# Optimization experiments

Hardware: AMD Instinct MI355X
Metric: run time of the kernel (lower is better)

Reference implementation:

```python
import jax, jax.numpy as jnp
import numpy as np

B, L, PD, DIM, H, DH, DEPTH, MLP, NIMG, NCLS, TH = 2, 2048, 768, 512, 8, 64, 2, 2048, 4, 1000, 32


def _ln(x, g):
    # bias-free LayerNorm (beta buffer is zeros), eps matches torch F.layer_norm
    mu = jnp.mean(x, axis=-1, keepdims=True)
    var = jnp.var(x, axis=-1, keepdims=True)
    return (x - mu) / jnp.sqrt(var + 1e-5) * g


def _rms(x, g):
    # F.normalize(dim=-1) * sqrt(dim_head) * gamma; x: [b,h,n,dh], g: [h,1,dh]
    n = jnp.linalg.norm(x, axis=-1, keepdims=True)
    return x / jnp.maximum(n, 1e-12) * (DH ** 0.5) * g


def _attn(x, context, mask, ln_g, qg, kg, Wq, Wkv, Wo):
    b, n = x.shape[0], x.shape[1]
    xn = _ln(x, ln_g)
    kv = xn if context is None else context  # context is NOT pre-normed (matches source)
    m = kv.shape[1]
    q = (xn @ Wq).reshape(b, n, H, DH).transpose(0, 2, 1, 3)   # [b,h,n,dh]
    k, v = jnp.split(kv @ Wkv, 2, axis=-1)
    k = k.reshape(b, m, H, DH).transpose(0, 2, 1, 3)
    v = v.reshape(b, m, H, DH).transpose(0, 2, 1, 3)
    q = _rms(q, qg)
    k = _rms(k, kg)
    dots = jnp.einsum('bhid,bhjd->bhij', q, k)  # no 1/sqrt(d): QK-RMSNorm carries the scale
    neg = -jnp.finfo(dots.dtype).max
    dots = jnp.where(mask, dots, neg)
    a = jax.nn.softmax(dots, axis=-1)
    out = jnp.einsum('bhij,bhjd->bhid', a, v)
    out = out.transpose(0, 2, 1, 3).reshape(b, n, H * DH)
    return out @ Wo


def _forward(patches, ln_pe1_g, W_pe, b_pe, ln_pe2_g, pos_h_emb, pos_w_emb,
             attn_ln_g, q_g, k_g, Wq, Wkv, Wo, ff_ln_g, W1, b1, W2, b2,
             final_ln_g, pool_q, pool_ln_g, pool_q_g, pool_k_g,
             pool_Wq, pool_Wkv, pool_Wo, head_ln_g, W_head,
             pos_h, pos_w, image_ids):
    # patch embedding: LN -> Linear -> LN, then factorized 2D pos embed
    x = _ln(patches, ln_pe1_g) @ W_pe + b_pe
    x = _ln(x, ln_pe2_g)
    x = x + pos_h_emb[pos_h] + pos_w_emb[pos_w]
    # block-diagonal attention mask: tokens attend only within their image
    mask = (image_ids[:, None, :, None] == image_ids[:, None, None, :])  # [B,1,L,L]
    for i in range(DEPTH):
        x = _attn(x, None, mask, attn_ln_g[i], q_g[i], k_g[i], Wq[i], Wkv[i], Wo[i]) + x
        h = _ln(x, ff_ln_g[i]) @ W1[i] + b1[i]
        h = jax.nn.gelu(h, approximate=False)
        x = h @ W2[i] + b2[i] + x
    x = _ln(x, final_ln_g)
    # attention pooling: one learned query per packed image
    queries = jnp.broadcast_to(pool_q, (B, NIMG, DIM))
    pmask = (jnp.arange(NIMG)[None, None, :, None] == image_ids[:, None, None, :])  # [B,1,NIMG,L]
    pooled = _attn(queries, x, pmask, pool_ln_g, pool_q_g, pool_k_g, pool_Wq, pool_Wkv, pool_Wo) + queries
    return _ln(pooled, head_ln_g) @ W_head  # [B, NIMG, NCLS]


def setup_inputs() -> dict:
    key = jax.random.key(0)
    ks = jax.random.split(key, 16)
    s = 0.02
    inp = {}
    inp['patches'] = jax.random.normal(ks[0], (B, L, PD), jnp.float32)
    inp['pos_h'] = jax.random.randint(ks[1], (B, L), 0, TH)
    inp['pos_w'] = jax.random.randint(ks[2], (B, L), 0, TH)
    inp['image_ids'] = jnp.sort(jax.random.randint(ks[3], (B, L), 0, NIMG), axis=-1)
    inp['ln_pe1_g'] = jnp.ones((PD,), jnp.float32)
    inp['W_pe'] = jax.random.normal(ks[4], (PD, DIM), jnp.float32) * s
    inp['b_pe'] = jnp.zeros((DIM,), jnp.float32)
    inp['ln_pe2_g'] = jnp.ones((DIM,), jnp.float32)
    inp['pos_h_emb'] = jax.random.normal(ks[5], (TH, DIM), jnp.float32)
    inp['pos_w_emb'] = jax.random.normal(ks[6], (TH, DIM), jnp.float32)
    inp['attn_ln_g'] = jnp.ones((DEPTH, DIM), jnp.float32)
    inp['q_g'] = jnp.ones((DEPTH, H, 1, DH), jnp.float32)
    inp['k_g'] = jnp.ones((DEPTH, H, 1, DH), jnp.float32)
    inp['Wq'] = jax.random.normal(ks[7], (DEPTH, DIM, H * DH), jnp.float32) * s
    inp['Wkv'] = jax.random.normal(ks[8], (DEPTH, DIM, 2 * H * DH), jnp.float32) * s
    inp['Wo'] = jax.random.normal(ks[9], (DEPTH, H * DH, DIM), jnp.float32) * s
    inp['ff_ln_g'] = jnp.ones((DEPTH, DIM), jnp.float32)
    inp['W1'] = jax.random.normal(ks[10], (DEPTH, DIM, MLP), jnp.float32) * s
    inp['b1'] = jnp.zeros((DEPTH, MLP), jnp.float32)
    inp['W2'] = jax.random.normal(ks[11], (DEPTH, MLP, DIM), jnp.float32) * s
    inp['b2'] = jnp.zeros((DEPTH, DIM), jnp.float32)
    inp['final_ln_g'] = jnp.ones((DIM,), jnp.float32)
    inp['pool_q'] = jax.random.normal(ks[12], (DIM,), jnp.float32)
    inp['pool_ln_g'] = jnp.ones((DIM,), jnp.float32)
    inp['pool_q_g'] = jnp.ones((H, 1, DH), jnp.float32)
    inp['pool_k_g'] = jnp.ones((H, 1, DH), jnp.float32)
    inp['pool_Wq'] = jax.random.normal(ks[13], (DIM, H * DH), jnp.float32) * s
    inp['pool_Wkv'] = jax.random.normal(ks[14], (DIM, 2 * H * DH), jnp.float32) * s
    inp['pool_Wo'] = jax.random.normal(ks[15], (H * DH, DIM), jnp.float32) * s
    inp['head_ln_g'] = jnp.ones((DIM,), jnp.float32)
    inp['W_head'] = jax.random.normal(jax.random.fold_in(key, 99), (DIM, NCLS), jnp.float32) * s
    return inp


def reference(patches, pos_h, pos_w, image_ids, ln_pe1_g, W_pe, b_pe, ln_pe2_g,
              pos_h_emb, pos_w_emb, attn_ln_g, q_g, k_g, Wq, Wkv, Wo, ff_ln_g,
              W1, b1, W2, b2, final_ln_g, pool_q, pool_ln_g, pool_q_g, pool_k_g,
              pool_Wq, pool_Wkv, pool_Wo, head_ln_g, W_head):
    return _forward(patches, ln_pe1_g, W_pe, b_pe, ln_pe2_g, pos_h_emb, pos_w_emb,
                    attn_ln_g, q_g, k_g, Wq, Wkv, Wo, ff_ln_g, W1, b1, W2, b2,
                    final_ln_g, pool_q, pool_ln_g, pool_q_g, pool_k_g,
                    pool_Wq, pool_Wkv, pool_Wo, head_ln_g, W_head,
                    pos_h, pos_w, image_ids)
```

## Files before the change

kernel.cpp:

```cpp
#include <hip/hip_runtime.h>
#include <hip/hip_bf16.h>
#include <cfloat>
#include <math.h>

#define BB 2
#define LL 2048
#define PD 768
#define DIM 512
#define HH 8
#define DH 64
#define DEPTH 2
#define MLP 2048
#define NIMG 4
#define NCLS 1000
#define ROWS (BB*LL)
#define QKV (3*DIM)
#define NEGBIG (-1e30f)

typedef __hip_bfloat16 bf16;
typedef __bf16 v8bf __attribute__((ext_vector_type(8)));
typedef float f32x4 __attribute__((ext_vector_type(4)));

__device__ __forceinline__ float ldin(const void* p, size_t i, int bf) {
    return bf ? __bfloat162float(((const bf16*)p)[i]) : ((const float*)p)[i];
}
__device__ __forceinline__ float lda(const float* p, size_t i) { return p[i]; }
__device__ __forceinline__ float lda(const bf16* p, size_t i) { return __bfloat162float(p[i]); }
__device__ __forceinline__ void st(float* p, size_t i, float v) { p[i] = v; }
__device__ __forceinline__ void st(bf16* p, size_t i, float v) { p[i] = __float2bfloat16(v); }
__device__ __forceinline__ unsigned short f2bf(float x) {
    return __builtin_bit_cast(unsigned short, __float2bfloat16(x));
}
__device__ __forceinline__ float us2f(unsigned short u) {
    return __bfloat162float(__builtin_bit_cast(bf16, u));
}

__device__ __forceinline__ void stage16(const void* gsrc, void* ldst)
{
    __builtin_amdgcn_global_load_lds(
        (const __attribute__((address_space(1))) unsigned int*)(unsigned long long)gsrc,
        (__attribute__((address_space(3))) unsigned int*)(unsigned int)(unsigned long long)ldst,
        16, 0, 0);
}

__global__ void detect_dtype_kernel(const void* ones, int* flag)
{
    if (threadIdx.x == 0 && blockIdx.x == 0)
        *flag = (((const unsigned*)ones)[0] == 0x3F803F80u) ? 1 : 0;
}

__global__ void wconv_kernel(const void* __restrict__ W, int K, int N, size_t inStride,
                             bf16* __restrict__ out, size_t outOff, size_t outStride,
                             const int* dtf)
{
    __shared__ float t[32][33];
    const int bf = *dtf;
    const size_t zin = (size_t)blockIdx.z * inStride;
    const size_t zout = outOff + (size_t)blockIdx.z * outStride;
    const int kb = blockIdx.y * 32, nb = blockIdx.x * 32;
    const int tx = threadIdx.x, ty = threadIdx.y;
    #pragma unroll
    for (int u = 0; u < 4; ++u)
        t[ty + 8 * u][tx] = ldin(W, zin + (size_t)(kb + ty + 8 * u) * N + nb + tx, bf);
    __syncthreads();
    #pragma unroll
    for (int u = 0; u < 4; ++u)
        out[zout + (size_t)(nb + ty + 8 * u) * K + kb + tx] = __float2bfloat16(t[tx][ty + 8 * u]);
}

template<int RAWIN, typename TOUT>
__global__ void ln_kernel(const void* __restrict__ in, const void* __restrict__ g, size_t goff,
                          TOUT* __restrict__ out, int D, const int* dtf)
{
    __shared__ float red[16];
    const int bf = *dtf;
    const int row = blockIdx.x, tid = threadIdx.x;
    const size_t base = (size_t)row * D;
    float s = 0.f, ss = 0.f;
    for (int d = tid; d < D; d += blockDim.x) {
        float v = RAWIN ? ldin(in, base + d, bf) : ((const float*)in)[base + d];
        s += v; ss += v * v;
    }
    for (int o = 32; o; o >>= 1) { s += __shfl_xor(s, o); ss += __shfl_xor(ss, o); }
    const int wid = tid >> 6, lane = tid & 63, nw = blockDim.x >> 6;
    if (lane == 0) { red[wid] = s; red[8 + wid] = ss; }
    __syncthreads();
    if (tid == 0) {
        float a = 0.f, b = 0.f;
        for (int w = 0; w < nw; ++w) { a += red[w]; b += red[8 + w]; }
        red[0] = a; red[8] = b;
    }
    __syncthreads();
    const float mean = red[0] / D;
    const float var  = red[8] / D - mean * mean;
    const float rstd = rsqrtf(var + 1e-5f);
    for (int d = tid; d < D; d += blockDim.x) {
        float v = RAWIN ? ldin(in, base + d, bf) : ((const float*)in)[base + d];
        st(out, base + d, (v - mean) * rstd * ldin(g, goff + d, bf));
    }
}

__global__ void patch_fuse_kernel(const float* __restrict__ part,
                                  const void* __restrict__ b_pe,
                                  const void* __restrict__ g1,
                                  const void* __restrict__ phe, const void* __restrict__ pwe,
                                  const int* __restrict__ ph, const int* __restrict__ pw,
                                  const void* __restrict__ g2,
                                  float* __restrict__ x, bf16* __restrict__ xb,
                                  const int* dtf)
{
    __shared__ float red[16];
    const int bf = *dtf;
    const int row = blockIdx.x, tid = threadIdx.x;
    const size_t base = (size_t)row * DIM;
    const int wid = tid >> 6, lane = tid & 63;
    float v[2];
    float s = 0.f, ss = 0.f;
    #pragma unroll
    for (int u = 0; u < 2; ++u) {
        const int d = tid + 256 * u;
        float a = part[base + d] + part[(size_t)ROWS * DIM + base + d] + ldin(b_pe, d, bf);
        v[u] = a; s += a; ss += a * a;
    }
    for (int o = 32; o; o >>= 1) { s += __shfl_xor(s, o); ss += __shfl_xor(ss, o); }
    if (lane == 0) { red[wid] = s; red[8 + wid] = ss; }
    __syncthreads();
    if (tid == 0) {
        float a = 0.f, b = 0.f;
        for (int w2 = 0; w2 < 4; ++w2) { a += red[w2]; b += red[8 + w2]; }
        red[0] = a; red[8] = b;
    }
    __syncthreads();
    {
        const float mean = red[0] / DIM;
        const float var  = red[8] / DIM - mean * mean;
        const float rstd = rsqrtf(var + 1e-5f);
        const size_t hoff = (size_t)ph[row] * DIM, woff = (size_t)pw[row] * DIM;
        s = 0.f; ss = 0.f;
        #pragma unroll
        for (int u = 0; u < 2; ++u) {
            const int d = tid + 256 * u;
            float a = (v[u] - mean) * rstd * ldin(g1, d, bf)
                    + ldin(phe, hoff + d, bf) + ldin(pwe, woff + d, bf);
            x[base + d] = a;
            v[u] = a; s += a; ss += a * a;
        }
    }
    for (int o = 32; o; o >>= 1) { s += __shfl_xor(s, o); ss += __shfl_xor(ss, o); }
    __syncthreads();
    if (lane == 0) { red[wid] = s; red[8 + wid] = ss; }
    __syncthreads();
    if (tid == 0) {
        float a = 0.f, b = 0.f;
        for (int w2 = 0; w2 < 4; ++w2) { a += red[w2]; b += red[8 + w2]; }
        red[0] = a; red[8] = b;
    }
    __syncthreads();
    const float mean = red[0] / DIM;
    const float var  = red[8] / DIM - mean * mean;
    const float rstd = rsqrtf(var + 1e-5f);
    #pragma unroll
    for (int u = 0; u < 2; ++u) {
        const int d = tid + 256 * u;
        xb[base + d] = __float2bfloat16((v[u] - mean) * rstd * ldin(g2, d, bf));
    }
}

#define GM 128
#define GN 64
#define GK 64

template<typename TO, int EPI>
__global__ void mgemm_kernel(const bf16* __restrict__ A, const bf16* __restrict__ Wt,
                             const void* __restrict__ bias, size_t boff,
                             const float* __restrict__ resid, TO* __restrict__ out,
                             int M, int N, int K, int kc, int gelu, const int* dtf)
{
    __shared__ __align__(16) unsigned short As[2][GM][GK];
    __shared__ __align__(16) unsigned short Bs[2][GN][GK];
    const int tid = threadIdx.x;
    const int w = tid >> 6, l = tid & 63, g = l >> 4, c = l & 15;
    const int wm = (w >> 1) * 64, wn = (w & 1) * 32;
    const int m0 = blockIdx.y * GM, n0 = blockIdx.x * GN;
    const int kbeg = blockIdx.z * kc;
    const int lrow = l >> 3, lcol = (l & 7) * 8;

#define STAGE_MG(BUF, K0)                                                          \
    {                                                                              \
        _Pragma("unroll")                                                          \
        for (int u = 0; u < 4; ++u) {                                              \
            const int rr = 32 * w + 8 * u;                                         \
            stage16(A + (size_t)(m0 + rr + lrow) * K + (K0) + lcol, &As[BUF][rr][0]); \
        }                                                                          \
        _Pragma("unroll")                                                          \
        for (int u = 0; u < 2; ++u) {                                              \
            const int rr = 16 * w + 8 * u;                                         \
            stage16(Wt + (size_t)(n0 + rr + lrow) * K + (K0) + lcol, &Bs[BUF][rr][0]); \
        }                                                                          \
    }

    f32x4 acc[4][2] = {};
    const int nt = kc / GK;
    STAGE_MG(0, kbeg);
    int cur = 0;
    for (int t = 0; t < nt; ++t) {
        if (t + 1 < nt) {
            STAGE_MG(cur ^ 1, kbeg + (t + 1) * GK);
            asm volatile("s_waitcnt vmcnt(6)" ::: "memory");
        } else {
            asm volatile("s_waitcnt vmcnt(0)" ::: "memory");
        }
        __builtin_amdgcn_s_barrier();
        __builtin_amdgcn_sched_barrier(0);
        #pragma unroll
        for (int kk = 0; kk < GK; kk += 32) {
            v8bf av[4], bv[2];
            #pragma unroll
            for (int i = 0; i < 4; ++i) av[i] = *(const v8bf*)&As[cur][wm + i * 16 + c][kk + 8 * g];
            #pragma unroll
            for (int j = 0; j < 2; ++j) bv[j] = *(const v8bf*)&Bs[cur][wn + j * 16 + c][kk + 8 * g];
            #pragma unroll
            for (int i = 0; i < 4; ++i)
                #pragma unroll
                for (int j = 0; j < 2; ++j)
                    acc[i][j] = __builtin_amdgcn_mfma_f32_16x16x32_bf16(av[i], bv[j], acc[i][j], 0, 0, 0);
        }
        __builtin_amdgcn_s_barrier();
        cur ^= 1;
    }
#undef STAGE_MG

    if (EPI == 0) {
        float* po = (float*)out + (size_t)blockIdx.z * M * N;
        #pragma unroll
        for (int i = 0; i < 4; ++i) {
            const int rb = m0 + wm + i * 16 + 4 * g;
            #pragma unroll
            for (int j = 0; j < 2; ++j) {
                const int col = n0 + wn + j * 16 + c;
                #pragma unroll
                for (int r = 0; r < 4; ++r)
                    po[(size_t)(rb + r) * N + col] = acc[i][j][r];
            }
        }
    } else {
        const int bf = *dtf;
        #pragma unroll
        for (int i = 0; i < 4; ++i) {
            const int rb = m0 + wm + i * 16 + 4 * g;
            #pragma unroll
            for (int j = 0; j < 2; ++j) {
                const int col = n0 + wn + j * 16 + c;
                const float bvl = bias ? ldin(bias, boff + col, bf) : 0.f;
                #pragma unroll
                for (int r = 0; r < 4; ++r) {
                    float v = acc[i][j][r] + bvl;
                    if (gelu) v = 0.5f * v * (1.f + erff(v * 0.70710678118654752f));
                    if (resid) v += resid[(size_t)(rb + r) * N + col];
                    st(out, (size_t)(rb + r) * N + col, v);
                }
            }
        }
    }
}

__global__ void comb_ln_kernel(const float* __restrict__ part, int S,
                               const void* __restrict__ bias, size_t boff,
                               float* __restrict__ x, const void* __restrict__ g, size_t goff,
                               bf16* __restrict__ xb, const int* dtf)
{
    __shared__ float red[16];
    const int bf = *dtf;
    const int row = blockIdx.x, tid = threadIdx.x;
    const size_t base = (size_t)row * DIM;
    float v[2];
    float s = 0.f, ss = 0.f;
    #pragma unroll
    for (int u = 0; u < 2; ++u) {
        const int d = tid + 256 * u;
        float a = 0.f;
        for (int sc = 0; sc < S; ++sc) a += part[(size_t)sc * ROWS * DIM + base + d];
        if (bias) a += ldin(bias, boff + d, bf);
        a += x[base + d];
        x[base + d] = a;
        v[u] = a; s += a; ss += a * a;
    }
    for (int o = 32; o; o >>= 1) { s += __shfl_xor(s, o); ss += __shfl_xor(ss, o); }
    const int wid = tid >> 6, lane = tid & 63;
    if (lane == 0) { red[wid] = s; red[8 + wid] = ss; }
    __syncthreads();
    if (tid == 0) {
        float a = 0.f, b = 0.f;
        for (int w2 = 0; w2 < 4; ++w2) { a += red[w2]; b += red[8 + w2]; }
        red[0] = a; red[8] = b;
    }
    __syncthreads();
    const float mean = red[0] / DIM;
    const float var  = red[8] / DIM - mean * mean;
    const float rstd = rsqrtf(var + 1e-5f);
    #pragma unroll
    for (int u = 0; u < 2; ++u) {
        const int d = tid + 256 * u;
        xb[base + d] = __float2bfloat16((v[u] - mean) * rstd * ldin(g, goff + d, bf));
    }
}

#define TS 16
template<typename TA, typename TO>
__global__ void gemm_kernel(const TA* __restrict__ A, const void* __restrict__ W, size_t woff,
                            const void* __restrict__ bias, size_t boff,
                            const float* __restrict__ resid, TO* __restrict__ out,
                            int M, int N, int K, int gelu, const int* dtf)
{
    __shared__ float As[TS][TS + 1];
    __shared__ float Bs[TS][TS + 1];
    const int bf = *dtf;
    const int tx = threadIdx.x, ty = threadIdx.y;
    const int col = blockIdx.x * TS + tx;
    const int row = blockIdx.y * TS + ty;
    float acc = 0.f;
    for (int k0 = 0; k0 < K; k0 += TS) {
        const int ka = k0 + tx;
        As[ty][tx] = (row < M && ka < K) ? lda(A, (size_t)row * K + ka) : 0.f;
        const int kb = k0 + ty;
        Bs[ty][tx] = (col < N && kb < K) ? ldin(W, woff + (size_t)kb * N + col, bf) : 0.f;
        __syncthreads();
        #pragma unroll
        for (int kk = 0; kk < TS; ++kk) acc = fmaf(As[ty][kk], Bs[kk][tx], acc);
        __syncthreads();
    }
    if (row < M && col < N) {
        if (bias) acc += ldin(bias, boff + col, bf);
        if (gelu) acc = 0.5f * acc * (1.f + erff(acc * 0.70710678118654752f));
        if (resid) acc += resid[(size_t)row * N + col];
        st(out, (size_t)row * N + col, acc);
    }
}

__global__ void rms_kernel(float* __restrict__ buf, const void* __restrict__ g, size_t goff,
                           int stride, int colbase, const int* dtf)
{
    const int bf = *dtf;
    const int r = blockIdx.x, h = blockIdx.y, lane = threadIdx.x;
    float* p = buf + (size_t)r * stride + colbase + h * DH;
    const float v = p[lane];
    float ss = v * v;
    for (int o = 32; o; o >>= 1) ss += __shfl_xor(ss, o);
    const float norm = sqrtf(ss);
    const float sc = 8.0f / fmaxf(norm, 1e-12f);
    p[lane] = v * sc * ldin(g, goff + h * DH + lane, bf);
}

__global__ void rms2_kernel(bf16* __restrict__ buf, int stride,
                            const void* __restrict__ g0, size_t g0off,
                            int base1, const void* __restrict__ g1, size_t g1off,
                            int nslot, const int* dtf)
{
    const int bf = *dtf;
    const int tid = threadIdx.x;
    const int s = tid >> 4, li = tid & 15;
    if (s >= nslot) return;
    const int h = s & 7;
    const int colbase = (s < 8) ? 0 : base1;
    const void* g = (s < 8) ? g0 : g1;
    const size_t go = ((s < 8) ? g0off : g1off) + h * DH + li * 4;
    bf16* p = buf + (size_t)blockIdx.x * stride + colbase + h * DH + li * 4;
    ushort4 v = *(const ushort4*)p;
    const float f0 = us2f(v.x), f1 = us2f(v.y), f2 = us2f(v.z), f3 = us2f(v.w);
    float ss = f0 * f0 + f1 * f1 + f2 * f2 + f3 * f3;
    ss += __shfl_xor(ss, 8); ss += __shfl_xor(ss, 4);
    ss += __shfl_xor(ss, 2); ss += __shfl_xor(ss, 1);
    const float sc = 8.0f / fmaxf(sqrtf(ss), 1e-12f);
    ushort4 o;
    o.x = f2bf(f0 * sc * ldin(g, go + 0, bf));
    o.y = f2bf(f1 * sc * ldin(g, go + 1, bf));
    o.z = f2bf(f2 * sc * ldin(g, go + 2, bf));
    o.w = f2bf(f3 * sc * ldin(g, go + 3, bf));
    *(ushort4*)p = o;
}

#define QT 64
#define KT 64
#define LP 72

__global__ void flash_attn_kernel(const bf16* __restrict__ q, int qstr,
                                  const bf16* __restrict__ kpt, const bf16* __restrict__ vpt,
                                  int kvstr, const int* __restrict__ ids,
                                  const void* __restrict__ qg, const void* __restrict__ kg,
                                  size_t goff, bf16* __restrict__ out, const int* dtf)
{
    __shared__ __align__(16) unsigned short Qs[QT][LP];
    __shared__ __align__(16) unsigned short Ks[KT][LP];
    __shared__ __align__(16) unsigned short Vt[DH][LP];
    __shared__ __align__(16) unsigned short Ps[QT][LP];
    __shared__ __align__(16) int ids_s[KT];
    __shared__ __align__(16) int qids_s[QT];
    __shared__ int range_s[2];

    const int bf = *dtf;
    const int tid = threadIdx.x;
    const int bid = blockIdx.x;
    const int s0 = (bid & 7) * 64 + (bid >> 3);
    const int qb = (s0 & 31) * QT;
    const int h = (s0 >> 5) & 7;
    const int b = s0 >> 8;
    const int w = tid >> 6, l = tid & 63, g = l >> 4, c = l & 15;

    const int r4 = tid >> 2, c16 = (tid & 3) << 4;

    float gk[16];
    #pragma unroll
    for (int j = 0; j < 16; ++j) gk[j] = ldin(kg, goff + h * DH + c16 + j, bf);

    {
        const bf16* qp = q + (size_t)(b * LL + qb + r4) * qstr + h * DH + c16;
        int4 raw0 = *(const int4*)qp;
        int4 raw1 = *(const int4*)(qp + 8);
        const unsigned short* u0 = (const unsigned short*)&raw0;
        const unsigned short* u1 = (const unsigned short*)&raw1;
        float f[16];
        float ssq = 0.f;
        #pragma unroll
        for (int j = 0; j < 8; ++j) { f[j] = us2f(u0[j]); f[8 + j] = us2f(u1[j]); }
        #pragma unroll
        for (int j = 0; j < 16; ++j) ssq += f[j] * f[j];
        ssq += __shfl_xor(ssq, 1); ssq += __shfl_xor(ssq, 2);
        const float sc = 8.0f / fmaxf(sqrtf(ssq), 1e-12f);
        ushort4 pk[4];
        unsigned short* pp = (unsigned short*)pk;
        #pragma unroll
        for (int j = 0; j < 16; ++j)
            pp[j] = f2bf(f[j] * sc * ldin(qg, goff + h * DH + c16 + j, bf));
        *(ushort4*)&Qs[r4][c16]      = pk[0];
        *(ushort4*)&Qs[r4][c16 + 4]  = pk[1];
        *(ushort4*)&Qs[r4][c16 + 8]  = pk[2];
        *(ushort4*)&Qs[r4][c16 + 12] = pk[3];
        if (tid < QT) qids_s[tid] = ids[b * LL + qb + tid];
    }
    if (tid == 0) {
        const int* bp = ids + b * LL;
        const int qlo = bp[qb], qhi = bp[qb + QT - 1];
        int lo = 0, hi = LL;
        while (lo < hi) { int mid = (lo + hi) >> 1; if (bp[mid] < qlo) lo = mid + 1; else hi = mid; }
        range_s[0] = lo;
        int lo2 = 0, hi2 = LL;
        while (lo2 < hi2) { int mid = (lo2 + hi2) >> 1; if (bp[mid] <= qhi) lo2 = mid + 1; else hi2 = mid; }
        range_s[1] = lo2;
    }
    __syncthreads();

    const int myid = qids_s[16 * w + c];
    const v8bf qf0 = *(const v8bf*)&Qs[16 * w + c][8 * g];
    const v8bf qf1 = *(const v8bf*)&Qs[16 * w + c][8 * g + 32];
    const int kb_start = (range_s[0] / KT) * KT;
    const int kb_end = range_s[1];

    f32x4 o[4];
    #pragma unroll
    for (int dt = 0; dt < 4; ++dt) o[dt] = (f32x4){0.f, 0.f, 0.f, 0.f};
    float mr = NEGBIG, lr = 0.f;

    for (int kb = kb_start; kb < kb_end; kb += KT) {
        __syncthreads();
        {
            const bf16* kp = kpt + (size_t)(b * LL + kb + r4) * kvstr + h * DH + c16;
            int4 raw0 = *(const int4*)kp;
            int4 raw1 = *(const int4*)(kp + 8);
            const unsigned short* u0 = (const unsigned short*)&raw0;
            const unsigned short* u1 = (const unsigned short*)&raw1;
            float f[16];
            float ssq = 0.f;
            #pragma unroll
            for (int j = 0; j < 8; ++j) { f[j] = us2f(u0[j]); f[8 + j] = us2f(u1[j]); }
            #pragma unroll
            for (int j = 0; j < 16; ++j) ssq += f[j] * f[j];
            ssq += __shfl_xor(ssq, 1); ssq += __shfl_xor(ssq, 2);
            const float sc = 8.0f / fmaxf(sqrtf(ssq), 1e-12f);
            ushort4 pk[4];
            unsigned short* pp = (unsigned short*)pk;
            #pragma unroll
            for (int j = 0; j < 16; ++j) pp[j] = f2bf(f[j] * sc * gk[j]);
            *(ushort4*)&Ks[r4][c16]      = pk[0];
            *(ushort4*)&Ks[r4][c16 + 4]  = pk[1];
            *(ushort4*)&Ks[r4][c16 + 8]  = pk[2];
            *(ushort4*)&Ks[r4][c16 + 12] = pk[3];
        }
        {
            const int kp2 = (tid & 31) * 2, db = (tid >> 5) * 8;
            const bf16* v0p = vpt + (size_t)(b * LL + kb + kp2) * kvstr + h * DH + db;
            const bf16* v1p = v0p + kvstr;
            const ushort4 a0 = *(const ushort4*)v0p;
            const ushort4 a1 = *(const ushort4*)(v0p + 4);
            const ushort4 b0 = *(const ushort4*)v1p;
            const ushort4 b1 = *(const ushort4*)(v1p + 4);
            const unsigned short* ap0 = (const unsigned short*)&a0;
            const unsigned short* ap1 = (const unsigned short*)&a1;
            const unsigned short* bp0 = (const unsigned short*)&b0;
            const unsigned short* bp1 = (const unsigned short*)&b1;
            #pragma unroll
            for (int j = 0; j < 4; ++j) {
                *(unsigned int*)&Vt[db + j][kp2]     = (unsigned)ap0[j] | ((unsigned)bp0[j] << 16);
                *(unsigned int*)&Vt[db + 4 + j][kp2] = (unsigned)ap1[j] | ((unsigned)bp1[j] << 16);
            }
        }
        if (tid < KT) ids_s[tid] = ids[b * LL + kb + tid];
        __syncthreads();

        f32x4 stt[4];
        __builtin_amdgcn_s_setprio(1);
        #pragma unroll
        for (int t = 0; t < 4; ++t) {
            stt[t] = (f32x4){0.f, 0.f, 0.f, 0.f};
            v8bf kf0 = *(const v8bf*)&Ks[16 * t + c][8 * g];
            v8bf kf1 = *(const v8bf*)&Ks[16 * t + c][8 * g + 32];
            stt[t] = __builtin_amdgcn_mfma_f32_16x16x32_bf16(kf0, qf0, stt[t], 0, 0, 0);
            stt[t] = __builtin_amdgcn_mfma_f32_16x16x32_bf16(kf1, qf1, stt[t], 0, 0, 0);
        }
        __builtin_amdgcn_s_setprio(0);

        float sv[16]; int mk[16];
        float tmax = NEGBIG;
        #pragma unroll
        for (int t = 0; t < 4; ++t) {
            int4 iv = *(const int4*)&ids_s[16 * t + 4 * g];
            const int* ivp = (const int*)&iv;
            #pragma unroll
            for (int r = 0; r < 4; ++r) {
                float s = stt[t][r];
                int m = (ivp[r] == myid);
                sv[4 * t + r] = s; mk[4 * t + r] = m;
                if (m) tmax = fmaxf(tmax, s);
            }
        }
        tmax = fmaxf(tmax, __shfl_xor(tmax, 16));
        tmax = fmaxf(tmax, __shfl_xor(tmax, 32));
        const float mnew = fmaxf(mr, tmax);
        const float al = __expf(mr - mnew);
        float tsum = 0.f;
        #pragma unroll
        for (int t = 0; t < 4; ++t) {
            ushort4 pk;
            unsigned short* pp = (unsigned short*)&pk;
            #pragma unroll
            for (int r = 0; r < 4; ++r) {
                float p = mk[4 * t + r] ? __expf(sv[4 * t + r] - mnew) : 0.f;
                tsum += p;
                pp[r] = f2bf(p);
            }
            *(ushort4*)&Ps[16 * w + c][16 * t + 4 * g] = pk;
        }
        tsum += __shfl_xor(tsum, 16);
        tsum += __shfl_xor(tsum, 32);
        lr = lr * al + tsum;
        mr = mnew;

        const float a0 = __shfl(al, 4 * g + 0);
        const float a1 = __shfl(al, 4 * g + 1);
        const float a2 = __shfl(al, 4 * g + 2);
        const float a3 = __shfl(al, 4 * g + 3);
        #pragma unroll
        for (int dt = 0; dt < 4; ++dt) {
            o[dt][0] *= a0; o[dt][1] *= a1; o[dt][2] *= a2; o[dt][3] *= a3;
        }

        const v8bf pf0 = *(const v8bf*)&Ps[16 * w + c][8 * g];
        const v8bf pf1 = *(const v8bf*)&Ps[16 * w + c][8 * g + 32];
        __builtin_amdgcn_s_setprio(1);
        #pragma unroll
        for (int dt = 0; dt < 4; ++dt) {
            v8bf vf0 = *(const v8bf*)&Vt[16 * dt + c][8 * g];
            v8bf vf1 = *(const v8bf*)&Vt[16 * dt + c][8 * g + 32];
            o[dt] = __builtin_amdgcn_mfma_f32_16x16x32_bf16(pf0, vf0, o[dt], 0, 0, 0);
            o[dt] = __builtin_amdgcn_mfma_f32_16x16x32_bf16(pf1, vf1, o[dt], 0, 0, 0);
        }
        __builtin_amdgcn_s_setprio(0);
    }

    const float li0 = 1.f / __shfl(lr, 4 * g + 0);
    const float li1 = 1.f / __shfl(lr, 4 * g + 1);
    const float li2 = 1.f / __shfl(lr, 4 * g + 2);
    const float li3 = 1.f / __shfl(lr, 4 * g + 3);
    #pragma unroll
    for (int dt = 0; dt < 4; ++dt) {
        bf16* op = out + (size_t)(b * LL + qb + 16 * w) * DIM + h * DH + 16 * dt + c;
        op[(size_t)(4 * g + 0) * DIM] = __float2bfloat16(o[dt][0] * li0);
        op[(size_t)(4 * g + 1) * DIM] = __float2bfloat16(o[dt][1] * li1);
        op[(size_t)(4 * g + 2) * DIM] = __float2bfloat16(o[dt][2] * li2);
        op[(size_t)(4 * g + 3) * DIM] = __float2bfloat16(o[dt][3] * li3);
    }
}

#define PCH 16
#define PCK (LL / PCH)

__global__ void pool_attn_part_kernel(const float* __restrict__ q, const bf16* __restrict__ kv,
                                      int kvs, const int* __restrict__ ids,
                                      float* __restrict__ ppm, float* __restrict__ ppl,
                                      float* __restrict__ ppo)
{
    const int iq = blockIdx.x & (NIMG - 1), ch = blockIdx.x >> 2;
    const int h = blockIdx.y, b = blockIdx.z;
    const int tid = threadIdx.x;
    const int qrow = b * NIMG + iq;
    const int j0 = ch * PCK;
    __shared__ float qs[DH];
    __shared__ float s[PCK];

    qs[tid] = q[(size_t)qrow * DIM + h * DH + tid];
    __syncthreads();
    #pragma unroll
    for (int u = 0; u < 2; ++u) {
        const int j = j0 + tid + 64 * u;
        const bf16* kp = kv + (size_t)(b * LL + j) * kvs + h * DH;
        float d = 0.f;
        #pragma unroll
        for (int t = 0; t < DH; t += 8) {
            int4 kvv = *(const int4*)&kp[t];
            const unsigned short* uu = (const unsigned short*)&kvv;
            #pragma unroll
            for (int z = 0; z < 8; ++z) d = fmaf(qs[t + z], us2f(uu[z]), d);
        }
        s[tid + 64 * u] = (ids[b * LL + j] == iq) ? d : NEGBIG;
    }
    __syncthreads();
    float m = fmaxf(s[tid], s[tid + 64]);
    for (int o = 32; o; o >>= 1) m = fmaxf(m, __shfl_xor(m, o));
    const float p0 = __expf(s[tid] - m), p1 = __expf(s[tid + 64] - m);
    float ls = p0 + p1;
    for (int o = 32; o; o >>= 1) ls += __shfl_xor(ls, o);
    s[tid] = p0; s[tid + 64] = p1;
    __syncthreads();
    float acc = 0.f;
    for (int jj = 0; jj < PCK; ++jj)
        acc += s[jj] * __bfloat162float(kv[(size_t)(b * LL + j0 + jj) * kvs + DIM + h * DH + tid]);
    const int p = ((b * HH + h) * NIMG + iq) * PCH + ch;
    if (tid == 0) { ppm[p] = m; ppl[p] = ls; }
    ppo[(size_t)p * DH + tid] = acc;
}

__global__ void pool_attn_comb_kernel(const float* __restrict__ ppm, const float* __restrict__ ppl,
                                      const float* __restrict__ ppo, float* __restrict__ out)
{
    const int iq = blockIdx.x, h = blockIdx.y, b = blockIdx.z;
    const int d = threadIdx.x;
    const int pb = ((b * HH + h) * NIMG + iq) * PCH;
    float mstar = NEGBIG;
    #pragma unroll
    for (int ch = 0; ch < PCH; ++ch) mstar = fmaxf(mstar, ppm[pb + ch]);
    float lsum = 0.f, osum = 0.f;
    #pragma unroll
    for (int ch = 0; ch < PCH; ++ch) {
        const float w = __expf(ppm[pb + ch] - mstar);
        lsum += ppl[pb + ch] * w;
        osum += ppo[(size_t)(pb + ch) * DH + d] * w;
    }
    out[(size_t)(b * NIMG + iq) * DIM + h * DH + d] = osum / lsum;
}

__global__ void fill_q_kernel(float* __restrict__ queries, const void* __restrict__ pool_q,
                              const int* dtf)
{
    const int bf = *dtf;
    const int idx = blockIdx.x * blockDim.x + threadIdx.x;
    if (idx < BB * NIMG * DIM) queries[idx] = ldin(pool_q, idx % DIM, bf);
}

__global__ void write_out_kernel(const float* __restrict__ in, void* __restrict__ out, int n,
                                 const int* dtf)
{
    const int bf = *dtf;
    const int idx = blockIdx.x * blockDim.x + threadIdx.x;
    if (idx < n) {
        if (bf) ((bf16*)out)[idx] = __float2bfloat16(in[idx]);
        else    ((float*)out)[idx] = in[idx];
    }
}

extern "C" void kernel_launch(void* const* d_in, const int* in_sizes, int n_in,
                              void* d_out, int out_size, void* d_ws, size_t ws_size,
                              hipStream_t stream)
{
    const void* patches   = d_in[0];
    const int*  pos_h     = (const int*) d_in[1];
    const int*  pos_w     = (const int*) d_in[2];
    const int*  image_ids = (const int*) d_in[3];
    const void* ln_pe1_g  = d_in[4];
    const void* W_pe      = d_in[5];
    const void* b_pe      = d_in[6];
    const void* ln_pe2_g  = d_in[7];
    const void* pos_h_emb = d_in[8];
    const void* pos_w_emb = d_in[9];
    const void* attn_ln_g = d_in[10];
    const void* q_g       = d_in[11];
    const void* k_g       = d_in[12];
    const void* Wq        = d_in[13];
    const void* Wkv       = d_in[14];
    const void* Wo        = d_in[15];
    const void* ff_ln_g   = d_in[16];
    const void* W1        = d_in[17];
    const void* b1        = d_in[18];
    const void* W2        = d_in[19];
    const void* b2        = d_in[20];
    const void* final_ln_g= d_in[21];
    const void* pool_q    = d_in[22];
    const void* pool_ln_g = d_in[23];
    const void* pool_q_g  = d_in[24];
    const void* pool_k_g  = d_in[25];
    const void* pool_Wq   = d_in[26];
    const void* pool_Wkv  = d_in[27];
    const void* pool_Wo   = d_in[28];
    const void* head_ln_g = d_in[29];
    const void* W_head    = d_in[30];

    char* p = (char*)d_ws;
    int* flag = (int*)p;                         p += 256;
    float* x   = (float*)p;                      p += (size_t)ROWS * DIM * 4;
    bf16* xb   = (bf16*)p;                       p += (size_t)ROWS * PD * 2;
    bf16* qkvb = (bf16*)p;  bf16* hb = qkvb;     p += (size_t)ROWS * MLP * 2;
    bf16* wpeT  = (bf16*)p;                      p += (size_t)DIM * PD * 2;
    bf16* wqkvT = (bf16*)p;                      p += (size_t)DEPTH * QKV * DIM * 2;
    bf16* woT   = (bf16*)p;                      p += (size_t)DEPTH * DIM * DIM * 2;
    bf16* w1T   = (bf16*)p;                      p += (size_t)DEPTH * MLP * DIM * 2;
    bf16* w2T   = (bf16*)p;                      p += (size_t)DEPTH * DIM * MLP * 2;
    bf16* pkvT  = (bf16*)p;                      p += (size_t)2 * DIM * DIM * 2;
    float* queries = (float*)p;                  p += 4096 * 4;
    float* qp      = (float*)p;                  p += 4096 * 4;
    float* pattn   = (float*)p;                  p += 4096 * 4;
    float* pooled  = (float*)p;                  p += 4096 * 4;
    bf16*  pln     = (bf16*)p;                   p += 4096 * 2;
    float* hout    = (float*)p;                  p += 8192 * 4;
    float* ppm     = (float*)p;                  p += 1024 * 4;
    float* ppl     = (float*)p;                  p += 1024 * 4;
    float* ppo     = (float*)p;                  p += (size_t)1024 * DH * 4;
    float* part    = (float*)p;                  p += (size_t)4 * ROWS * DIM * 4;

    const dim3 blk256(256);
    const dim3 blkG(TS, TS);
    const dim3 blkT(32, 8);

    detect_dtype_kernel<<<1, 1, 0, stream>>>(ln_pe1_g, flag);

    wconv_kernel<<<dim3(DIM / 32, PD / 32, 1), blkT, 0, stream>>>(
        W_pe, PD, DIM, 0, wpeT, 0, 0, flag);
    wconv_kernel<<<dim3(DIM / 32, DIM / 32, DEPTH), blkT, 0, stream>>>(
        Wq, DIM, DIM, (size_t)DIM * DIM, wqkvT, 0, (size_t)QKV * DIM, flag);
    wconv_kernel<<<dim3(2 * DIM / 32, DIM / 32, DEPTH), blkT, 0, stream>>>(
        Wkv, DIM, 2 * DIM, (size_t)DIM * 2 * DIM, wqkvT, (size_t)DIM * DIM, (size_t)QKV * DIM, flag);
    wconv_kernel<<<dim3(DIM / 32, DIM / 32, DEPTH), blkT, 0, stream>>>(
        Wo, DIM, DIM, (size_t)DIM * DIM, woT, 0, (size_t)DIM * DIM, flag);
    wconv_kernel<<<dim3(MLP / 32, DIM / 32, DEPTH), blkT, 0, stream>>>(
        W1, DIM, MLP, (size_t)DIM * MLP, w1T, 0, (size_t)MLP * DIM, flag);
    wconv_kernel<<<dim3(DIM / 32, MLP / 32, DEPTH), blkT, 0, stream>>>(
        W2, MLP, DIM, (size_t)MLP * DIM, w2T, 0, (size_t)DIM * MLP, flag);
    wconv_kernel<<<dim3(2 * DIM / 32, DIM / 32, 1), blkT, 0, stream>>>(
        pool_Wkv, DIM, 2 * DIM, 0, pkvT, 0, 0, flag);

    ln_kernel<1, bf16><<<ROWS, blk256, 0, stream>>>(patches, ln_pe1_g, 0, xb, PD, flag);
    mgemm_kernel<float, 0><<<dim3(DIM / GN, ROWS / GM, 2), blk256, 0, stream>>>(
        xb, wpeT, nullptr, 0, nullptr, part, ROWS, DIM, PD, PD / 2, 0, flag);
    patch_fuse_kernel<<<ROWS, blk256, 0, stream>>>(
        part, b_pe, ln_pe2_g, pos_h_emb, pos_w_emb, pos_h, pos_w, attn_ln_g, x, xb, flag);

    for (int i = 0; i < DEPTH; ++i) {
        mgemm_kernel<bf16, 1><<<dim3(QKV / GN, ROWS / GM, 1), blk256, 0, stream>>>(
            xb, wqkvT + (size_t)i * QKV * DIM, nullptr, 0, nullptr, qkvb,
            ROWS, QKV, DIM, DIM, 0, flag);
        flash_attn_kernel<<<dim3(512), blk256, 0, stream>>>(
            qkvb, QKV, qkvb + DIM, qkvb + 2 * DIM, QKV, image_ids,
            q_g, k_g, (size_t)i * HH * DH, xb, flag);
        mgemm_kernel<float, 0><<<dim3(DIM / GN, ROWS / GM, 2), blk256, 0, stream>>>(
            xb, woT + (size_t)i * DIM * DIM, nullptr, 0, nullptr, part,
            ROWS, DIM, DIM, DIM / 2, 0, flag);
        comb_ln_kernel<<<ROWS, blk256, 0, stream>>>(
            part, 2, nullptr, 0, x, ff_ln_g, (size_t)i * DIM, xb, flag);
        mgemm_kernel<bf16, 1><<<dim3(MLP / GN, ROWS / GM, 1), blk256, 0, stream>>>(
            xb, w1T + (size_t)i * MLP * DIM, b1, (size_t)i * MLP, nullptr, hb,
            ROWS, MLP, DIM, DIM, 1, flag);
        mgemm_kernel<float, 0><<<dim3(DIM / GN, ROWS / GM, 4), blk256, 0, stream>>>(
            hb, w2T + (size_t)i * DIM * MLP, nullptr, 0, nullptr, part,
            ROWS, DIM, MLP, MLP / 4, 0, flag);
        const void* gnext = (i + 1 < DEPTH) ? attn_ln_g : final_ln_g;
        const size_t gnoff = (i + 1 < DEPTH) ? (size_t)(i + 1) * DIM : 0;
        comb_ln_kernel<<<ROWS, blk256, 0, stream>>>(
            part, 4, b2, (size_t)i * DIM, x, gnext, gnoff, xb, flag);
    }

    fill_q_kernel<<<(BB * NIMG * DIM + 255) / 256, blk256, 0, stream>>>(queries, pool_q, flag);
    ln_kernel<0, bf16><<<BB * NIMG, blk256, 0, stream>>>(queries, pool_ln_g, 0, pln, DIM, flag);
    gemm_kernel<bf16, float><<<dim3(DIM / TS, 1), blkG, 0, stream>>>(
        pln, pool_Wq, 0, nullptr, 0, nullptr, qp, BB * NIMG, DIM, DIM, 0, flag);
    mgemm_kernel<bf16, 1><<<dim3(2 * DIM / GN, ROWS / GM, 1), blk256, 0, stream>>>(
        xb, pkvT, nullptr, 0, nullptr, qkvb, ROWS, 2 * DIM, DIM, DIM, 0, flag);
    rms_kernel<<<dim3(BB * NIMG, HH), dim3(64), 0, stream>>>(
        qp, pool_q_g, 0, DIM, 0, flag);
    rms2_kernel<<<ROWS, blk256, 0, stream>>>(
        qkvb, 2 * DIM, pool_k_g, 0, 0, nullptr, 0, 8, flag);
    pool_attn_part_kernel<<<dim3(NIMG * PCH, HH, BB), dim3(64), 0, stream>>>(
        qp, qkvb, 2 * DIM, image_ids, ppm, ppl, ppo);
    pool_attn_comb_kernel<<<dim3(NIMG, HH, BB), dim3(64), 0, stream>>>(ppm, ppl, ppo, pattn);
    gemm_kernel<float, float><<<dim3(DIM / TS, 1), blkG, 0, stream>>>(
        pattn, pool_Wo, 0, nullptr, 0, queries, pooled, BB * NIMG, DIM, DIM, 0, flag);

    ln_kernel<0, bf16><<<BB * NIMG, blk256, 0, stream>>>(pooled, head_ln_g, 0, pln, DIM, flag);
    gemm_kernel<bf16, float><<<dim3((NCLS + TS - 1) / TS, 1), blkG, 0, stream>>>(
        pln, W_head, 0, nullptr, 0, nullptr, hout, BB * NIMG, NCLS, DIM, 0, flag);
    write_out_kernel<<<(BB * NIMG * NCLS + 255) / 256, blk256, 0, stream>>>(
        hout, d_out, BB * NIMG * NCLS, flag);
}
```

Before: 463.8 us.

## Split flash attention key range in two with a separate combine kernel

The flash attention kernel now splits each query tile's key range into two halves, handled by separate blocks (1024 instead of 512), each writing unnormalized partial outputs plus running max and sum to fp32 scratch. A new combine kernel merges the two partials with log-sum-exp weighting and writes bf16 output. This raises parallelism to fill more CUs on the MI355X. The cost is an extra launch and fp32 partial-output traffic through the reused `part` buffer. rms2_kernel is also simplified by dropping its unused second-slot parameters.

```diff
diff --git a/kernel.cpp b/kernel.cpp
--- a/kernel.cpp
+++ b/kernel.cpp
@@ -16,6 +16,8 @@
 #define ROWS (BB*LL)
 #define QKV (3*DIM)
 #define NEGBIG (-1e30f)
+#define BHL (BB*HH*LL)
+#define BHLD ((size_t)BHL*DH)
 
 typedef __hip_bfloat16 bf16;
 typedef __bf16 v8bf __attribute__((ext_vector_type(8)));
@@ -352,19 +354,15 @@
 }
 
 __global__ void rms2_kernel(bf16* __restrict__ buf, int stride,
-                            const void* __restrict__ g0, size_t g0off,
-                            int base1, const void* __restrict__ g1, size_t g1off,
-                            int nslot, const int* dtf)
+                            const void* __restrict__ g0, size_t g0off, int nslot, const int* dtf)
 {
     const int bf = *dtf;
     const int tid = threadIdx.x;
     const int s = tid >> 4, li = tid & 15;
     if (s >= nslot) return;
     const int h = s & 7;
-    const int colbase = (s < 8) ? 0 : base1;
-    const void* g = (s < 8) ? g0 : g1;
-    const size_t go = ((s < 8) ? g0off : g1off) + h * DH + li * 4;
-    bf16* p = buf + (size_t)blockIdx.x * stride + colbase + h * DH + li * 4;
+    const size_t go = g0off + h * DH + li * 4;
+    bf16* p = buf + (size_t)blockIdx.x * stride + h * DH + li * 4;
     ushort4 v = *(const ushort4*)p;
     const float f0 = us2f(v.x), f1 = us2f(v.y), f2 = us2f(v.z), f3 = us2f(v.w);
     float ss = f0 * f0 + f1 * f1 + f2 * f2 + f3 * f3;
@@ -372,10 +370,10 @@
     ss += __shfl_xor(ss, 2); ss += __shfl_xor(ss, 1);
     const float sc = 8.0f / fmaxf(sqrtf(ss), 1e-12f);
     ushort4 o;
-    o.x = f2bf(f0 * sc * ldin(g, go + 0, bf));
-    o.y = f2bf(f1 * sc * ldin(g, go + 1, bf));
-    o.z = f2bf(f2 * sc * ldin(g, go + 2, bf));
-    o.w = f2bf(f3 * sc * ldin(g, go + 3, bf));
+    o.x = f2bf(f0 * sc * ldin(g0, go + 0, bf));
+    o.y = f2bf(f1 * sc * ldin(g0, go + 1, bf));
+    o.z = f2bf(f2 * sc * ldin(g0, go + 2, bf));
+    o.w = f2bf(f3 * sc * ldin(g0, go + 3, bf));
     *(ushort4*)p = o;
 }
 
@@ -383,11 +381,12 @@
 #define KT 64
 #define LP 72
 
-__global__ void flash_attn_kernel(const bf16* __restrict__ q, int qstr,
+__global__ void flash_part_kernel(const bf16* __restrict__ q, int qstr,
                                   const bf16* __restrict__ kpt, const bf16* __restrict__ vpt,
                                   int kvstr, const int* __restrict__ ids,
                                   const void* __restrict__ qg, const void* __restrict__ kg,
-                                  size_t goff, bf16* __restrict__ out, const int* dtf)
+                                  size_t goff, float* __restrict__ pm, float* __restrict__ pl,
+                                  float* __restrict__ po, const int* dtf)
 {
     __shared__ __align__(16) unsigned short Qs[QT][LP];
     __shared__ __align__(16) unsigned short Ks[KT][LP];
@@ -400,10 +399,11 @@
     const int bf = *dtf;
     const int tid = threadIdx.x;
     const int bid = blockIdx.x;
-    const int s0 = (bid & 7) * 64 + (bid >> 3);
-    const int qb = (s0 & 31) * QT;
-    const int h = (s0 >> 5) & 7;
-    const int b = s0 >> 8;
+    const int s0 = (bid & 7) * 128 + (bid >> 3);
+    const int half = s0 & 1;
+    const int qb = ((s0 >> 1) & 31) * QT;
+    const int h = (s0 >> 6) & 7;
+    const int b = s0 >> 9;
     const int w = tid >> 6, l = tid & 63, g = l >> 4, c = l & 15;
 
     const int r4 = tid >> 2, c16 = (tid & 3) << 4;
@@ -452,8 +452,12 @@
     const int myid = qids_s[16 * w + c];
     const v8bf qf0 = *(const v8bf*)&Qs[16 * w + c][8 * g];
     const v8bf qf1 = *(const v8bf*)&Qs[16 * w + c][8 * g + 32];
-    const int kb_start = (range_s[0] / KT) * KT;
-    const int kb_end = range_s[1];
+    const int ts = (range_s[0] / KT) * KT;
+    const int te = range_s[1];
+    const int ntile = (te - ts + KT - 1) / KT;
+    const int h0 = (ntile + 1) >> 1;
+    const int kb_start = ts + (half ? h0 * KT : 0);
+    const int kb_end = half ? te : ((ts + h0 * KT) < te ? (ts + h0 * KT) : te);
 
     f32x4 o[4];
     #pragma unroll
@@ -576,18 +580,35 @@
         __builtin_amdgcn_s_setprio(0);
     }
 
-    const float li0 = 1.f / __shfl(lr, 4 * g + 0);
-    const float li1 = 1.f / __shfl(lr, 4 * g + 1);
-    const float li2 = 1.f / __shfl(lr, 4 * g + 2);
-    const float li3 = 1.f / __shfl(lr, 4 * g + 3);
+    const size_t qbase = (size_t)(b * HH + h) * LL + qb;
+    if (g == 0) {
+        pm[(size_t)half * BHL + qbase + 16 * w + c] = mr;
+        pl[(size_t)half * BHL + qbase + 16 * w + c] = lr;
+    }
     #pragma unroll
     for (int dt = 0; dt < 4; ++dt) {
-        bf16* op = out + (size_t)(b * LL + qb + 16 * w) * DIM + h * DH + 16 * dt + c;
-        op[(size_t)(4 * g + 0) * DIM] = __float2bfloat16(o[dt][0] * li0);
-        op[(size_t)(4 * g + 1) * DIM] = __float2bfloat16(o[dt][1] * li1);
-        op[(size_t)(4 * g + 2) * DIM] = __float2bfloat16(o[dt][2] * li2);
-        op[(size_t)(4 * g + 3) * DIM] = __float2bfloat16(o[dt][3] * li3);
-    }
+        float* op = po + (size_t)half * BHLD + (qbase + 16 * w) * DH + 16 * dt + c;
+        op[(size_t)(4 * g + 0) * DH] = o[dt][0];
+        op[(size_t)(4 * g + 1) * DH] = o[dt][1];
+        op[(size_t)(4 * g + 2) * DH] = o[dt][2];
+        op[(size_t)(4 * g + 3) * DH] = o[dt][3];
+    }
+}
+
+__global__ void flash_comb_kernel(const float* __restrict__ pm, const float* __restrict__ pl,
+                                  const float* __restrict__ po, bf16* __restrict__ out)
+{
+    const int h = blockIdx.y, b = blockIdx.z;
+    const int qrow = blockIdx.x * 4 + (threadIdx.x >> 6);
+    const int d = threadIdx.x & 63;
+    const size_t qg = (size_t)(b * HH + h) * LL + qrow;
+    const float m0 = pm[qg], m1 = pm[BHL + qg];
+    const float l0 = pl[qg], l1 = pl[BHL + qg];
+    const float ms = fmaxf(m0, m1);
+    const float w0 = __expf(m0 - ms), w1 = __expf(m1 - ms);
+    const float num = w0 * po[qg * DH + d] + w1 * po[BHLD + qg * DH + d];
+    const float den = w0 * l0 + w1 * l1;
+    out[((size_t)b * LL + qrow) * DIM + h * DH + d] = __float2bfloat16(num / den);
 }
 
 #define PCH 16
@@ -732,7 +753,10 @@
     float* ppm     = (float*)p;                  p += 1024 * 4;
     float* ppl     = (float*)p;                  p += 1024 * 4;
     float* ppo     = (float*)p;                  p += (size_t)1024 * DH * 4;
+    float* pm      = (float*)p;                  p += (size_t)2 * BHL * 4;
+    float* pl      = (float*)p;                  p += (size_t)2 * BHL * 4;
     float* part    = (float*)p;                  p += (size_t)4 * ROWS * DIM * 4;
+    float* po      = part;
 
     const dim3 blk256(256);
     const dim3 blkG(TS, TS);
@@ -765,9 +789,10 @@
         mgemm_kernel<bf16, 1><<<dim3(QKV / GN, ROWS / GM, 1), blk256, 0, stream>>>(
             xb, wqkvT + (size_t)i * QKV * DIM, nullptr, 0, nullptr, qkvb,
             ROWS, QKV, DIM, DIM, 0, flag);
-        flash_attn_kernel<<<dim3(512), blk256, 0, stream>>>(
+        flash_part_kernel<<<dim3(1024), blk256, 0, stream>>>(
             qkvb, QKV, qkvb + DIM, qkvb + 2 * DIM, QKV, image_ids,
-            q_g, k_g, (size_t)i * HH * DH, xb, flag);
+            q_g, k_g, (size_t)i * HH * DH, pm, pl, po, flag);
+        flash_comb_kernel<<<dim3(LL / 4, HH, BB), blk256, 0, stream>>>(pm, pl, po, xb);
         mgemm_kernel<float, 0><<<dim3(DIM / GN, ROWS / GM, 2), blk256, 0, stream>>>(
             xb, woT + (size_t)i * DIM * DIM, nullptr, 0, nullptr, part,
             ROWS, DIM, DIM, DIM / 2, 0, flag);
@@ -793,8 +818,7 @@
         xb, pkvT, nullptr, 0, nullptr, qkvb, ROWS, 2 * DIM, DIM, DIM, 0, flag);
     rms_kernel<<<dim3(BB * NIMG, HH), dim3(64), 0, stream>>>(
         qp, pool_q_g, 0, DIM, 0, flag);
-    rms2_kernel<<<ROWS, blk256, 0, stream>>>(
-        qkvb, 2 * DIM, pool_k_g, 0, 0, nullptr, 0, 8, flag);
+    rms2_kernel<<<ROWS, blk256, 0, stream>>>(qkvb, 2 * DIM, pool_k_g, 0, 8, flag);
     pool_attn_part_kernel<<<dim3(NIMG * PCH, HH, BB), dim3(64), 0, stream>>>(
         qp, qkvb, 2 * DIM, image_ids, ppm, ppl, ppo);
     pool_attn_comb_kernel<<<dim3(NIMG, HH, BB), dim3(64), 0, stream>>>(ppm, ppl, ppo, pattn);
```

Result: no change. 466.1 us (+0.5%).
